# Kernel tuning notes

Measured on AMD Instinct MI355X. Metric: run time of the kernel, lower is better.

## Reference

```python
import jax, jax.numpy as jnp
import numpy as np

BETA = 0.25

def setup_inputs() -> dict:
    key = jax.random.key(0)
    k1, k2 = jax.random.split(key)
    N, K, D = 32768, 8192, 512
    latents = jax.random.normal(k1, (N, D), dtype=jnp.float32)
    # torch init: uniform(-1/num_protos, 1/num_protos)
    prototypes = jax.random.uniform(k2, (K, D), dtype=jnp.float32, minval=-1.0 / K, maxval=1.0 / K)
    return {"latents": latents, "prototypes": prototypes}


def reference(latents, prototypes):
    dists = (jnp.sum(latents ** 2, axis=1, keepdims=True)
             + jnp.sum(prototypes ** 2, axis=1)
             - 2.0 * jnp.matmul(latents, prototypes.T))
    closest = jnp.argmin(dists, axis=1)  # [N]
    # one-hot @ prototypes == gather (same math, no NxK intermediate)
    quantized = prototypes[closest]  # [N, D]
    commitment_loss = jnp.mean((jax.lax.stop_gradient(quantized) - latents) ** 2)
    embedding_loss = jnp.mean((quantized - jax.lax.stop_gradient(latents)) ** 2)
    vq_loss = commitment_loss * BETA + embedding_loss
    # straight-through estimator
    quantized_st = latents + jax.lax.stop_gradient(quantized - latents)
    return quantized_st, vq_loss
```

## Files before the change

kernel.cpp:

```cpp
#include <hip/hip_runtime.h>


#define N_ROWS 32768
#define K_PROTO 8192
#define DIM 512
#define BM 128
#define BN 128
#define BKB 128
#define GROUPS 8
#define TILES 8

typedef unsigned char u8;
typedef unsigned int u32;
typedef __attribute__((ext_vector_type(4))) int i32x4;
typedef __attribute__((ext_vector_type(8))) int i32x8;
typedef __attribute__((ext_vector_type(4))) float f32x4;

__device__ __forceinline__ void async16(const void* g, void* s) {
    __builtin_amdgcn_global_load_lds(
        (const __attribute__((address_space(1))) void*)g,
        (__attribute__((address_space(3))) void*)s, 16, 0, 0);
}

__device__ __forceinline__ int pk4(float a, float b, float c, float d) {
    int v = 0;
    v = __builtin_amdgcn_cvt_pk_fp8_f32(a, b, v, false);
    v = __builtin_amdgcn_cvt_pk_fp8_f32(c, d, v, true);
    return v;
}

__global__ void __launch_bounds__(256) conv_latents(const float* __restrict__ X,
                                                    u8* __restrict__ Xf,
                                                    u32* __restrict__ best) {
    if (blockIdx.x < 128) best[blockIdx.x * 256 + threadIdx.x] = 0xFFFFFFFFu;
    size_t i = ((size_t)blockIdx.x * 256 + threadIdx.x) * 16;
    float4 a = ((const float4*)(X + i))[0];
    float4 b = ((const float4*)(X + i))[1];
    float4 c = ((const float4*)(X + i))[2];
    float4 d = ((const float4*)(X + i))[3];
    int4 o;
    o.x = pk4(a.x, a.y, a.z, a.w);
    o.y = pk4(b.x, b.y, b.z, b.w);
    o.z = pk4(c.x, c.y, c.z, c.w);
    o.w = pk4(d.x, d.y, d.z, d.w);
    *(int4*)(Xf + i) = o;
}

__global__ void __launch_bounds__(256) conv_protos(const float* __restrict__ P,
                                                   u8* __restrict__ Pf,
                                                   float* __restrict__ pnC) {
    int row  = blockIdx.x * 4 + (threadIdx.x >> 6);
    int lane = threadIdx.x & 63;
    const float* src = P + (size_t)row * DIM + lane * 8;
    float4 a = ((const float4*)src)[0];
    float4 b = ((const float4*)src)[1];
    int2 o;
    o.x = pk4(a.x * 8192.0f, a.y * 8192.0f, a.z * 8192.0f, a.w * 8192.0f);
    o.y = pk4(b.x * 8192.0f, b.y * 8192.0f, b.z * 8192.0f, b.w * 8192.0f);
    *(int2*)(Pf + (size_t)row * DIM + lane * 8) = o;
    float ss = a.x*a.x + a.y*a.y + a.z*a.z + a.w*a.w
             + b.x*b.x + b.y*b.y + b.z*b.z + b.w*b.w;
    #pragma unroll
    for (int off = 32; off; off >>= 1) ss += __shfl_down(ss, off);
    if (lane == 0) pnC[row] = ss * 8192.0f + 256.0f;
}

__global__ void __launch_bounds__(256, 3) vq_score_kernel(const u8* __restrict__ Xf,
                                                          const u8* __restrict__ Pf,
                                                          const float* __restrict__ pnC,
                                                          u32* __restrict__ best) {
    __shared__ u8 As[BM * BKB];
    __shared__ u8 Bs[BN * BKB];

    const int tid  = threadIdx.x;
    const int row0 = blockIdx.x * BM;
    const int colg = blockIdx.y * (TILES * BN);

    const int w    = tid >> 6, lane = tid & 63;
    const int quad = lane >> 4, l15 = lane & 15;

    const u8* gA[4]; u8* sA[4];
    const u8* pB[4]; u8* sB[4];
    #pragma unroll
    for (int i = 0; i < 4; i++) {
        int f = tid + i * 256;
        int row = f >> 3, c = (f & 7) ^ (row & 7);
        gA[i] = Xf + (size_t)(row0 + row) * DIM + c * 16;
        sA[i] = As + f * 16;
        pB[i] = Pf + (size_t)(colg + row) * DIM + c * 16;
        sB[i] = Bs + f * 16;
    }

    const int x7   = l15 & 7;
    const int pos0 = (quad ^ x7) * 16;
    const int pos1 = pos0 ^ 64;
    const u8* Arow = &As[(w * 32 + l15) * BKB];
    const u8* Brow = &Bs[l15 * BKB];

    u32 v[2][4];
    #pragma unroll
    for (int i = 0; i < 2; i++)
        #pragma unroll
        for (int r = 0; r < 4; r++) v[i][r] = 0xFFFFFFFFu;

    for (int t = 0; t < TILES; ++t) {
        f32x4 acc[2][8];
        #pragma unroll
        for (int i = 0; i < 2; i++)
            #pragma unroll
            for (int j = 0; j < 8; j++) acc[i][j] = (f32x4)0.0f;

        for (int kt = 0; kt < DIM / BKB; ++kt) {
            const int k0 = kt * BKB;
            #pragma unroll
            for (int i = 0; i < 4; i++) {
                async16(gA[i] + k0, sA[i]);
                async16(pB[i] + k0, sB[i]);
            }
            __syncthreads();

            i32x8 a0 = __builtin_shufflevector(*(const i32x4*)(Arow + pos0),
                                               *(const i32x4*)(Arow + pos1),
                                               0, 1, 2, 3, 4, 5, 6, 7);
            i32x8 a1 = __builtin_shufflevector(*(const i32x4*)(Arow + 16 * BKB + pos0),
                                               *(const i32x4*)(Arow + 16 * BKB + pos1),
                                               0, 1, 2, 3, 4, 5, 6, 7);
            #pragma unroll
            for (int tn = 0; tn < 8; tn++) {
                i32x8 b = __builtin_shufflevector(
                    *(const i32x4*)(Brow + tn * 16 * BKB + pos0),
                    *(const i32x4*)(Brow + tn * 16 * BKB + pos1),
                    0, 1, 2, 3, 4, 5, 6, 7);
                acc[0][tn] = __builtin_amdgcn_mfma_scale_f32_16x16x128_f8f6f4(
                    a0, b, acc[0][tn], 0, 0, 0, 127, 0, 127);
                acc[1][tn] = __builtin_amdgcn_mfma_scale_f32_16x16x128_f8f6f4(
                    a1, b, acc[1][tn], 0, 0, 0, 127, 0, 127);
            }
            __syncthreads();
        }

        #pragma unroll
        for (int tn = 0; tn < 8; tn++) {
            const u32 kidx = (u32)(colg + t * BN + tn * 16 + l15);
            float pc = pnC[kidx];
            #pragma unroll
            for (int tm = 0; tm < 2; tm++)
                #pragma unroll
                for (int r = 0; r < 4; r++) {
                    float sk = fmaf(-2.0f, acc[tm][tn][r], pc);
                    u32 key = (__float_as_uint(sk) & 0xFFFFE000u) | kidx;
                    if (key < v[tm][r]) v[tm][r] = key;
                }
        }
        #pragma unroll
        for (int i = 0; i < 4; i++) pB[i] += (size_t)BN * DIM;
    }

    #pragma unroll
    for (int tm = 0; tm < 2; tm++)
        #pragma unroll
        for (int r = 0; r < 4; r++) {
            u32 x = v[tm][r];
            #pragma unroll
            for (int off = 1; off < 16; off <<= 1) {
                u32 o = (u32)__shfl_xor((int)x, off);
                if (o < x) x = o;
            }
            if (l15 == 0)
                atomicMin(&best[row0 + w * 32 + tm * 16 + quad * 4 + r], x);
        }
}

__global__ void __launch_bounds__(128) vq_gather_kernel(const float* __restrict__ X,
                                                        const float* __restrict__ P,
                                                        const u32* __restrict__ best,
                                                        float* __restrict__ out,
                                                        float* __restrict__ partial) {
    const int n = blockIdx.x, t = threadIdx.x;
    const u32 k = best[n] & (K_PROTO - 1);
    const float4 p = ((const float4*)(P + (size_t)k * DIM))[t];
    const float4 x = ((const float4*)(X + (size_t)n * DIM))[t];
    ((float4*)(out + (size_t)n * DIM))[t] = p;
    float dx = p.x - x.x, dy = p.y - x.y, dz = p.z - x.z, dw = p.w - x.w;
    float ss = dx * dx + dy * dy + dz * dz + dw * dw;
    #pragma unroll
    for (int off = 32; off; off >>= 1) ss += __shfl_down(ss, off);
    __shared__ float part[2];
    if ((t & 63) == 0) part[t >> 6] = ss;
    __syncthreads();
    if (t == 0) partial[n] = part[0] + part[1];
}

__global__ void __launch_bounds__(256) loss_reduce(const float* __restrict__ partial,
                                                   float* __restrict__ out) {
    const int t = threadIdx.x;
    float s = 0.0f;
    #pragma unroll
    for (int i = 0; i < 32; i++) {
        float4 a = ((const float4*)partial)[t * 32 + i];
        s += a.x + a.y + a.z + a.w;
    }
    #pragma unroll
    for (int off = 32; off; off >>= 1) s += __shfl_down(s, off);
    __shared__ float part[4];
    if ((t & 63) == 0) part[t >> 6] = s;
    __syncthreads();
    if (t == 0)
        out[(size_t)N_ROWS * DIM] =
            (part[0] + part[1] + part[2] + part[3]) * 7.450580596923828e-08f;
}

extern "C" void kernel_launch(void* const* d_in, const int* in_sizes, int n_in,
                              void* d_out, int out_size, void* d_ws, size_t ws_size,
                              hipStream_t stream) {
    const float* X = (const float*)d_in[0];
    const float* P = (const float*)d_in[1];
    float* out = (float*)d_out;
    char* ws = (char*)d_ws;

    u8* Xf = (u8*)ws;
    u8* Pf = (u8*)(ws + 16777216);
    float* pnC = (float*)(ws + 20971520);
    u32* best = (u32*)(ws + 21004288);
    float* partial = (float*)(ws + 21135360);

    conv_latents<<<dim3(4096), dim3(256), 0, stream>>>(X, Xf, best);
    conv_protos<<<dim3(2048), dim3(256), 0, stream>>>(P, Pf, pnC);
    vq_score_kernel<<<dim3(N_ROWS / BM, GROUPS), dim3(256), 0, stream>>>(Xf, Pf, pnC, best);
    vq_gather_kernel<<<dim3(N_ROWS), dim3(128), 0, stream>>>(X, P, best, out, partial);
    loss_reduce<<<dim3(1), dim3(256), 0, stream>>>(partial, out);
}
```

Baseline: 290.1 us.

## Keep A fragments in registers and triple-buffer B tiles with async prefetch

```diff
diff --git a/kernel.cpp b/kernel.cpp
--- a/kernel.cpp
+++ b/kernel.cpp
@@ -9,6 +9,8 @@
 #define BKB 128
 #define GROUPS 8
 #define TILES 8
+#define NSTEP 32
+#define BUFB 16384
 
 typedef unsigned char u8;
 typedef unsigned int u32;
@@ -65,12 +67,24 @@
     if (lane == 0) pnC[row] = ss * 8192.0f + 256.0f;
 }
 
+__device__ __forceinline__ void stage_b(const u8* __restrict__ Pf, u8* BsF,
+                                        int s2, int colg, const int (&voff)[4],
+                                        int tid) {
+    const int t2 = s2 >> 2, kt2 = s2 & 3, sb = s2 % 3;
+    const u8* src = Pf + (size_t)(colg + t2 * BN) * DIM + kt2 * BKB;
+    u8* dst = BsF + sb * BUFB + tid * 16;
+    #pragma unroll
+    for (int i = 0; i < 4; i++)
+        async16(src + voff[i], dst + i * 4096);
+}
+
 __global__ void __launch_bounds__(256, 3) vq_score_kernel(const u8* __restrict__ Xf,
                                                           const u8* __restrict__ Pf,
                                                           const float* __restrict__ pnC,
                                                           u32* __restrict__ best) {
-    __shared__ u8 As[BM * BKB];
-    __shared__ u8 Bs[BN * BKB];
+    __shared__ __align__(16) u8 lds_raw[3 * BUFB + 4096];
+    u8* BsF = lds_raw;
+    const float* pcs = (const float*)(lds_raw + 3 * BUFB);
 
     const int tid  = threadIdx.x;
     const int row0 = blockIdx.x * BM;
@@ -79,23 +93,49 @@
     const int w    = tid >> 6, lane = tid & 63;
     const int quad = lane >> 4, l15 = lane & 15;
 
-    const u8* gA[4]; u8* sA[4];
-    const u8* pB[4]; u8* sB[4];
+    int voff[4];
     #pragma unroll
     for (int i = 0; i < 4; i++) {
         int f = tid + i * 256;
         int row = f >> 3, c = (f & 7) ^ (row & 7);
-        gA[i] = Xf + (size_t)(row0 + row) * DIM + c * 16;
-        sA[i] = As + f * 16;
-        pB[i] = Pf + (size_t)(colg + row) * DIM + c * 16;
-        sB[i] = Bs + f * 16;
+        voff[i] = row * DIM + c * 16;
     }
 
     const int x7   = l15 & 7;
-    const int pos0 = (quad ^ x7) * 16;
+    const int pos0 = (quad ^ x7) << 4;
     const int pos1 = pos0 ^ 64;
-    const u8* Arow = &As[(w * 32 + l15) * BKB];
-    const u8* Brow = &Bs[l15 * BKB];
+
+    i32x8 a[4][2];
+    #pragma unroll
+    for (int r = 0; r < 2; r++) {
+        #pragma unroll
+        for (int i = 0; i < 8; i++) {
+            int f = tid + i * 256;
+            int sl = f >> 10;
+            int fi = f & 1023;
+            int row = fi >> 3, c = (fi & 7) ^ (row & 7);
+            async16(Xf + (size_t)(row0 + row) * DIM + (2 * r + sl) * BKB + c * 16,
+                    BsF + f * 16);
+        }
+        if (r == 0)
+            async16((const u8*)(pnC + colg) + tid * 16, lds_raw + 3 * BUFB + tid * 16);
+        __syncthreads();
+        #pragma unroll
+        for (int sl = 0; sl < 2; sl++) {
+            const u8* Ar = BsF + sl * BUFB + (w * 32 + l15) * BKB;
+            #pragma unroll
+            for (int tm = 0; tm < 2; tm++) {
+                const u8* p = Ar + tm * 16 * BKB;
+                a[2 * r + sl][tm] = __builtin_shufflevector(
+                    *(const i32x4*)(p + pos0), *(const i32x4*)(p + pos1),
+                    0, 1, 2, 3, 4, 5, 6, 7);
+            }
+        }
+        __syncthreads();
+    }
+
+    stage_b(Pf, BsF, 0, colg, voff, tid);
+    stage_b(Pf, BsF, 1, colg, voff, tid);
 
     u32 v[2][4];
     #pragma unroll
@@ -110,39 +150,38 @@
             #pragma unroll
             for (int j = 0; j < 8; j++) acc[i][j] = (f32x4)0.0f;
 
-        for (int kt = 0; kt < DIM / BKB; ++kt) {
-            const int k0 = kt * BKB;
-            #pragma unroll
-            for (int i = 0; i < 4; i++) {
-                async16(gA[i] + k0, sA[i]);
-                async16(pB[i] + k0, sB[i]);
-            }
-            __syncthreads();
-
-            i32x8 a0 = __builtin_shufflevector(*(const i32x4*)(Arow + pos0),
-                                               *(const i32x4*)(Arow + pos1),
-                                               0, 1, 2, 3, 4, 5, 6, 7);
-            i32x8 a1 = __builtin_shufflevector(*(const i32x4*)(Arow + 16 * BKB + pos0),
-                                               *(const i32x4*)(Arow + 16 * BKB + pos1),
-                                               0, 1, 2, 3, 4, 5, 6, 7);
+        #pragma unroll
+        for (int kt = 0; kt < 4; ++kt) {
+            const int s = t * 4 + kt;
+            if (kt == 3 && t == TILES - 1)
+                asm volatile("s_waitcnt vmcnt(0)" ::: "memory");
+            else
+                asm volatile("s_waitcnt vmcnt(4)" ::: "memory");
+            __builtin_amdgcn_s_barrier();
+            __builtin_amdgcn_sched_barrier(0);
+
+            if (s + 2 < NSTEP) stage_b(Pf, BsF, s + 2, colg, voff, tid);
+
+            const u8* Brow = BsF + (s % 3) * BUFB + l15 * BKB;
             #pragma unroll
             for (int tn = 0; tn < 8; tn++) {
+                const u8* bp = Brow + tn * 16 * BKB;
                 i32x8 b = __builtin_shufflevector(
-                    *(const i32x4*)(Brow + tn * 16 * BKB + pos0),
-                    *(const i32x4*)(Brow + tn * 16 * BKB + pos1),
+                    *(const i32x4*)(bp + pos0), *(const i32x4*)(bp + pos1),
                     0, 1, 2, 3, 4, 5, 6, 7);
                 acc[0][tn] = __builtin_amdgcn_mfma_scale_f32_16x16x128_f8f6f4(
-                    a0, b, acc[0][tn], 0, 0, 0, 127, 0, 127);
+                    a[kt][0], b, acc[0][tn], 0, 0, 0, 127, 0, 127);
                 acc[1][tn] = __builtin_amdgcn_mfma_scale_f32_16x16x128_f8f6f4(
-                    a1, b, acc[1][tn], 0, 0, 0, 127, 0, 127);
+                    a[kt][1], b, acc[1][tn], 0, 0, 0, 127, 0, 127);
             }
-            __syncthreads();
+            __builtin_amdgcn_sched_barrier(0);
         }
 
         #pragma unroll
         for (int tn = 0; tn < 8; tn++) {
-            const u32 kidx = (u32)(colg + t * BN + tn * 16 + l15);
-            float pc = pnC[kidx];
+            const int ci = t * BN + tn * 16 + l15;
+            const float pc = pcs[ci];
+            const u32 kidx = (u32)(colg + ci);
             #pragma unroll
             for (int tm = 0; tm < 2; tm++)
                 #pragma unroll
@@ -152,8 +191,6 @@
                     if (key < v[tm][r]) v[tm][r] = key;
                 }
         }
-        #pragma unroll
-        for (int i = 0; i < 4; i++) pB[i] += (size_t)BN * DIM;
     }
 
     #pragma unroll
```

Result: slower. 510.4 us (+75.9%).

## Double-buffer LDS tiles with prefetch and stage prototype norms in shared memory

Applied to the files above, without the earlier changes.

```diff
diff --git a/kernel.cpp b/kernel.cpp
--- a/kernel.cpp
+++ b/kernel.cpp
@@ -9,6 +9,9 @@
 #define BKB 128
 #define GROUPS 8
 #define TILES 8
+#define NSTEP 32
+#define BUFA 16384
+#define BUFBB 16384
 
 typedef unsigned char u8;
 typedef unsigned int u32;
@@ -65,12 +68,13 @@
     if (lane == 0) pnC[row] = ss * 8192.0f + 256.0f;
 }
 
-__global__ void __launch_bounds__(256, 3) vq_score_kernel(const u8* __restrict__ Xf,
+__global__ void __launch_bounds__(256, 2) vq_score_kernel(const u8* __restrict__ Xf,
                                                           const u8* __restrict__ Pf,
                                                           const float* __restrict__ pnC,
                                                           u32* __restrict__ best) {
-    __shared__ u8 As[BM * BKB];
-    __shared__ u8 Bs[BN * BKB];
+    __shared__ __align__(16) u8 As[2 * BUFA];
+    __shared__ __align__(16) u8 Bs[2 * BUFBB];
+    __shared__ __align__(16) float pcs[TILES * BN];
 
     const int tid  = threadIdx.x;
     const int row0 = blockIdx.x * BM;
@@ -79,23 +83,29 @@
     const int w    = tid >> 6, lane = tid & 63;
     const int quad = lane >> 4, l15 = lane & 15;
 
-    const u8* gA[4]; u8* sA[4];
-    const u8* pB[4]; u8* sB[4];
+    const u8* gA[4]; const u8* gB[4]; int sOff[4];
     #pragma unroll
     for (int i = 0; i < 4; i++) {
         int f = tid + i * 256;
         int row = f >> 3, c = (f & 7) ^ (row & 7);
         gA[i] = Xf + (size_t)(row0 + row) * DIM + c * 16;
-        sA[i] = As + f * 16;
-        pB[i] = Pf + (size_t)(colg + row) * DIM + c * 16;
-        sB[i] = Bs + f * 16;
+        gB[i] = Pf + (size_t)(colg + row) * DIM + c * 16;
+        sOff[i] = f * 16;
     }
 
     const int x7   = l15 & 7;
-    const int pos0 = (quad ^ x7) * 16;
+    const int pos0 = (quad ^ x7) << 4;
     const int pos1 = pos0 ^ 64;
-    const u8* Arow = &As[(w * 32 + l15) * BKB];
-    const u8* Brow = &Bs[l15 * BKB];
+
+    {
+        #pragma unroll
+        for (int i = 0; i < 4; i++) {
+            async16(gA[i], As + sOff[i]);
+            async16(gB[i], Bs + sOff[i]);
+        }
+        async16((const u8*)(pnC + colg) + tid * 16, (u8*)pcs + tid * 16);
+    }
+    __syncthreads();
 
     u32 v[2][4];
     #pragma unroll
@@ -110,14 +120,25 @@
             #pragma unroll
             for (int j = 0; j < 8; j++) acc[i][j] = (f32x4)0.0f;
 
-        for (int kt = 0; kt < DIM / BKB; ++kt) {
-            const int k0 = kt * BKB;
-            #pragma unroll
-            for (int i = 0; i < 4; i++) {
-                async16(gA[i] + k0, sA[i]);
-                async16(pB[i] + k0, sB[i]);
+        #pragma unroll
+        for (int kt = 0; kt < 4; ++kt) {
+            const int s = t * 4 + kt;
+
+            if (s + 1 < NSTEP) {
+                const int kt2 = (s + 1) & 3;
+                const size_t tOff = (size_t)((s + 1) >> 2) * BN * DIM;
+                u8* dA = As + ((s + 1) & 1) * BUFA;
+                u8* dB = Bs + ((s + 1) & 1) * BUFBB;
+                #pragma unroll
+                for (int i = 0; i < 4; i++) {
+                    async16(gA[i] + kt2 * BKB, dA + sOff[i]);
+                    async16(gB[i] + tOff + kt2 * BKB, dB + sOff[i]);
+                }
             }
-            __syncthreads();
+            __builtin_amdgcn_sched_barrier(0);
+
+            const u8* Arow = As + (s & 1) * BUFA + (w * 32 + l15) * BKB;
+            const u8* Brow = Bs + (s & 1) * BUFBB + l15 * BKB;
 
             i32x8 a0 = __builtin_shufflevector(*(const i32x4*)(Arow + pos0),
                                                *(const i32x4*)(Arow + pos1),
@@ -125,24 +146,27 @@
             i32x8 a1 = __builtin_shufflevector(*(const i32x4*)(Arow + 16 * BKB + pos0),
                                                *(const i32x4*)(Arow + 16 * BKB + pos1),
                                                0, 1, 2, 3, 4, 5, 6, 7);
+            __builtin_amdgcn_s_setprio(1);
             #pragma unroll
             for (int tn = 0; tn < 8; tn++) {
+                const u8* bp = Brow + tn * 16 * BKB;
                 i32x8 b = __builtin_shufflevector(
-                    *(const i32x4*)(Brow + tn * 16 * BKB + pos0),
-                    *(const i32x4*)(Brow + tn * 16 * BKB + pos1),
+                    *(const i32x4*)(bp + pos0), *(const i32x4*)(bp + pos1),
                     0, 1, 2, 3, 4, 5, 6, 7);
                 acc[0][tn] = __builtin_amdgcn_mfma_scale_f32_16x16x128_f8f6f4(
                     a0, b, acc[0][tn], 0, 0, 0, 127, 0, 127);
                 acc[1][tn] = __builtin_amdgcn_mfma_scale_f32_16x16x128_f8f6f4(
                     a1, b, acc[1][tn], 0, 0, 0, 127, 0, 127);
             }
+            __builtin_amdgcn_s_setprio(0);
             __syncthreads();
         }
 
         #pragma unroll
         for (int tn = 0; tn < 8; tn++) {
-            const u32 kidx = (u32)(colg + t * BN + tn * 16 + l15);
-            float pc = pnC[kidx];
+            const int ci = t * BN + tn * 16 + l15;
+            const float pc = pcs[ci];
+            const u32 kidx = (u32)(colg + ci);
             #pragma unroll
             for (int tm = 0; tm < 2; tm++)
                 #pragma unroll
@@ -152,8 +176,6 @@
                     if (key < v[tm][r]) v[tm][r] = key;
                 }
         }
-        #pragma unroll
-        for (int i = 0; i < 4; i++) pB[i] += (size_t)BN * DIM;
     }
 
     #pragma unroll
```

New measurement: 339.5 us. +17.0%, slower.
